# Kernel optimization log

Measured on AMD Instinct MI355X. Metric: run time of the kernel, lower is better.

## Reference

```python
import jax, jax.numpy as jnp
import numpy as np
from jax import lax

N_G, E_G, E_LG = 100000, 400000, 1200000
N_T, E_T, E_LGT = 50000, 100000, 300000
D_F, D_MSG_G = 64, 128
VOCAB, D_EMB, D_MSG_T = 780, 128, 128
N_ITERS_G, N_ITERS_T = 4, 4
SCALE = 0.05  # keep relu/sum chains numerically tame over iterations


def setup_inputs() -> dict:
    key = jax.random.key(0)
    ks = jax.random.split(key, 32)
    f32 = jnp.float32
    w = lambda k, sh: jax.random.normal(k, sh, f32) * SCALE
    return {
        "G_f": jax.random.normal(ks[0], (N_G, D_F), f32),
        "G_ef": jax.random.normal(ks[1], (E_G, D_F), f32),
        "G_src": jax.random.randint(ks[2], (E_G,), 0, N_G, jnp.int32),
        "G_dst": jax.random.randint(ks[3], (E_G,), 0, N_G, jnp.int32),
        "G_lg_src": jax.random.randint(ks[4], (E_LG,), 0, E_G, jnp.int32),
        "G_lg_dst": jax.random.randint(ks[5], (E_LG,), 0, E_G, jnp.int32),
        "T_id": jax.random.randint(ks[6], (N_T,), 0, VOCAB, jnp.int32),
        "T_src": jax.random.randint(ks[7], (E_T,), 0, N_T, jnp.int32),
        "T_dst": jax.random.randint(ks[8], (E_T,), 0, N_T, jnp.int32),
        "T_lg_src": jax.random.randint(ks[9], (E_LGT,), 0, E_T, jnp.int32),
        "T_lg_dst": jax.random.randint(ks[10], (E_LGT,), 0, E_T, jnp.int32),
        "embeddings": jax.random.normal(ks[11], (VOCAB, D_EMB), f32),
        "W1": w(ks[12], (D_F, D_MSG_G)),
        "W2": w(ks[13], (D_F, D_MSG_G)),
        "W3": w(ks[14], (D_MSG_G, D_MSG_G)),
        "U1_G": w(ks[15], (D_F, D_MSG_G)),
        "U2_G": w(ks[16], (D_MSG_G, D_MSG_G)),
        "Wz": w(ks[17], (D_EMB, D_MSG_T)),
        "Uz": w(ks[18], (D_MSG_T, D_MSG_T)),
        "Wr": w(ks[19], (D_EMB, D_MSG_T)),
        "Ur": w(ks[20], (D_MSG_T, D_MSG_T)),
        "Wh": w(ks[21], (D_EMB, D_MSG_T)),
        "Uh": w(ks[22], (D_MSG_T, D_MSG_T)),
        "U1_T": w(ks[23], (D_EMB, D_MSG_T)),
        "U2_T": w(ks[24], (D_MSG_T, D_MSG_T)),
    }


def reference(G_f, G_ef, G_src, G_dst, G_lg_src, G_lg_dst,
              T_id, T_src, T_dst, T_lg_src, T_lg_dst,
              embeddings, W1, W2, W3, U1_G, U2_G,
              Wz, Uz, Wr, Ur, Wh, Uh, U1_T, U2_T):
    seg = jax.ops.segment_sum

    # ---- molecule graph G: loopy-BP MLP messages on the line graph ----
    f_src_G = G_f[G_src]                               # [E_G, D_F] copy_src
    base_G = f_src_G @ W1 + G_ef @ W2                  # loop-invariant part of g1_G

    def stepG(msg, _):
        sum_msg = seg(msg[G_lg_src], G_lg_dst, num_segments=E_G)
        return jax.nn.relu(base_G + sum_msg @ W3), None

    msgG0 = jnp.zeros((E_G, D_MSG_G), G_f.dtype)
    msgG, _ = lax.scan(stepG, msgG0, None, length=N_ITERS_G)

    # readout g2_G: sum edge msgs into dst nodes
    sG = seg(msgG, G_dst, num_segments=N_G)
    x_G = jax.nn.relu(G_f @ U1_G + sG @ U2_G)          # [N_G, D_MSG_G]

    # ---- junction tree T: GRU messages on the tree line graph ----
    f_T = embeddings[T_id]                             # one-hot id @ embeddings
    f_src_T = f_T[T_src]                               # [E_T, D_EMB]
    xz, xr, xh = f_src_T @ Wz, f_src_T @ Wr, f_src_T @ Wh

    def stepT(msg, _):
        s = seg(msg[T_lg_src], T_lg_dst, num_segments=E_T)
        z = jax.nn.sigmoid(xz + s @ Uz)
        r = jax.nn.sigmoid(xr + s @ Ur)
        h = jnp.tanh(xh + (r * s) @ Uh)
        return (1.0 - z) * s + z * h, None

    msgT0 = jnp.zeros((E_T, D_MSG_T), f_T.dtype)
    msgT, _ = lax.scan(stepT, msgT0, None, length=N_ITERS_T)

    sT = seg(msgT, T_dst, num_segments=N_T)
    x_T = jax.nn.relu(f_T @ U1_T + sT @ U2_T)          # [N_T, D_MSG_T]

    # concat node readouts (same width) so output is a single array
    return jnp.concatenate([x_G, x_T], axis=0)         # [N_G+N_T, 128]
```

## Files before the change

kernel.cpp:

```cpp
#include <hip/hip_runtime.h>

#define NG 100000
#define EG 400000
#define ELG 1200000
#define NT 50000
#define ET 100000
#define ELGT 300000

#define GEG ((EG + 63) / 64)
#define GET ((ET + 63) / 64)
#define GNG ((NG + 63) / 64)
#define GNT ((NT + 63) / 64)

#define SEG1 EG
#define SEG2 (EG + NG)
#define SEG3 (EG + NG + ET)
#define NSEG_ALL (EG + NG + ET + NT)
#define NE_ALL (ELG + EG + ELGT + ET)

typedef unsigned short u16;
typedef unsigned int u32;
typedef __attribute__((ext_vector_type(8))) short bf16x8;
typedef __attribute__((ext_vector_type(4))) float f32x4;

#define TILE_BYTES (64 * 256)

__device__ __forceinline__ float bflo(u32 p){ return __uint_as_float(p << 16); }
__device__ __forceinline__ float bfhi(u32 p){ return __uint_as_float(p & 0xffff0000u); }
__device__ __forceinline__ float bf2f(u16 h){ return __uint_as_float(((u32)h) << 16); }
__device__ __forceinline__ u16 f2bf(float f){
  u32 u = __float_as_uint(f);
  u32 r = u + 0x7fffu + ((u >> 16) & 1u);
  return (u16)(r >> 16);
}
__device__ __forceinline__ float sigm(float x){ return 1.0f / (1.0f + __expf(-x)); }
__device__ __forceinline__ float tanh_(float x){ return 2.0f / (1.0f + __expf(-2.0f * x)) - 1.0f; }
__device__ __forceinline__ float relu_(float x){ return x > 0.0f ? x : 0.0f; }

__device__ __forceinline__ int swz(int r, int c){ return r * 256 + (c ^ ((r & 7) << 4)); }

__device__ __forceinline__ void zero8(float v[8]){
  #pragma unroll
  for (int j = 0; j < 8; j++) v[j] = 0.f;
}
__device__ __forceinline__ uint4 pack8(const float v[8]){
  uint4 o;
  o.x = f2bf(v[0]) | ((u32)f2bf(v[1]) << 16);
  o.y = f2bf(v[2]) | ((u32)f2bf(v[3]) << 16);
  o.z = f2bf(v[4]) | ((u32)f2bf(v[5]) << 16);
  o.w = f2bf(v[6]) | ((u32)f2bf(v[7]) << 16);
  return o;
}
__device__ __forceinline__ uint2 pack4(const f32x4& a){
  uint2 o;
  o.x = (u32)f2bf(a[0]) | ((u32)f2bf(a[1]) << 16);
  o.y = (u32)f2bf(a[2]) | ((u32)f2bf(a[3]) << 16);
  return o;
}

__global__ void k_sniff(const u32* __restrict__ g, int* __restrict__ flag){
  __shared__ int sh[2];
  if (threadIdx.x < 2) sh[threadIdx.x] = 0;
  __syncthreads();
  int c0 = 0, c1 = 0;
  for (int i = 0; i < 16; i++){
    u32 w = g[threadIdx.x * 16 + i];
    u32 lo = w & 0xFFFFu;
    if (lo == 0u) c0++;
    else { u32 e = (lo >> 7) & 0xFFu; if (e >= 96u && e <= 144u) c1++; }
  }
  atomicAdd(&sh[0], c0); atomicAdd(&sh[1], c1);
  __syncthreads();
  if (threadIdx.x == 0) *flag = (sh[0] < 512 && sh[1] > 2048) ? 1 : 0;
}

__global__ void k_cvt_all(const void* p0, const void* p1, const void* p2, const void* p3,
                          const void* p4, const void* p5, const void* p6, const void* p7,
                          const void* p8, const void* p9, const void* p10, const void* p11,
                          const void* p12, float* __restrict__ wm, const int* __restrict__ flagp){
  int i = blockIdx.x * 256 + threadIdx.x;
  if (i >= 188416) return;
  const int offs[14] = {0,8192,16384,32768,40960,57344,73728,90112,106496,122880,139264,155648,172032,188416};
  const void* ps[13] = {p0,p1,p2,p3,p4,p5,p6,p7,p8,p9,p10,p11,p12};
  int w = 0;
  while (i >= offs[w + 1]) w++;
  int li = i - offs[w];
  wm[i] = (*flagp) ? bf2f(((const u16*)ps[w])[li]) : ((const float*)ps[w])[li];
}

__global__ void k_mkfrag_all(const float* __restrict__ wm, u16* __restrict__ frag){
  const int wmo[13] = {0,8192,16384,32768,40960,57344,73728,90112,106496,122880,139264,155648,172032};
  const int nks[13] = {2,2,4,2,4,4,4,4,4,4,4,4,4};
  int b = blockIdx.x;
  int wi = 0, ks = b;
  while (ks >= nks[wi]){ ks -= nks[wi]; wi++; }
  const float* W = wm + wmo[wi];
  int nt = threadIdx.x >> 6, lane = threadIdx.x & 63;
  int kr = ks * 32 + ((lane >> 4) << 3);
  int col = nt * 16 + (lane & 15);
  u16* o = frag + (size_t)b * 4096 + nt * 512 + lane * 8;
  #pragma unroll
  for (int j = 0; j < 8; j++) o[j] = f2bf(W[(size_t)(kr + j) * 128 + col]);
}

__device__ __forceinline__ const void* rowdt(const void* mat, size_t row, int W, int bf){
  return bf ? (const void*)((const u16*)mat + row * (size_t)W)
            : (const void*)((const float*)mat + row * (size_t)W);
}
__device__ __forceinline__ void load8(const void* rowbase, int c8, int bf, float v[8]){
  if (bf){
    uint4 d = ((const uint4*)rowbase)[c8];
    v[0]=bflo(d.x); v[1]=bfhi(d.x); v[2]=bflo(d.y); v[3]=bfhi(d.y);
    v[4]=bflo(d.z); v[5]=bfhi(d.z); v[6]=bflo(d.w); v[7]=bfhi(d.w);
  } else {
    const float4* p = (const float4*)rowbase + (c8 << 1);
    float4 a = p[0], b = p[1];
    v[0]=a.x; v[1]=a.y; v[2]=a.z; v[3]=a.w; v[4]=b.x; v[5]=b.y; v[6]=b.z; v[7]=b.w;
  }
}

__global__ void k_hist_all(const int* __restrict__ Glgd, const int* __restrict__ Gd,
                           const int* __restrict__ Tlgd, const int* __restrict__ Td,
                           int* __restrict__ cnt){
  int e = blockIdx.x * 256 + threadIdx.x;
  if (e >= NE_ALL) return;
  int seg;
  if (e < ELG)                       seg = Glgd[e];
  else if (e < ELG + EG)             seg = SEG1 + Gd[e - ELG];
  else if (e < ELG + EG + ELGT)      seg = SEG2 + Tlgd[e - ELG - EG];
  else                               seg = SEG3 + Td[e - ELG - EG - ELGT];
  atomicAdd(&cnt[seg], 1);
}

__global__ void k_scan1(const int* __restrict__ cnt, int n, int* __restrict__ csum){
  int base = blockIdx.x * 4096, tid = threadIdx.x;
  int s = 0;
  for (int i = 0; i < 16; i++){ int idx = base + i * 256 + tid; if (idx < n) s += cnt[idx]; }
  __shared__ int red[4];
  for (int off = 32; off; off >>= 1) s += __shfl_down(s, off, 64);
  if ((tid & 63) == 0) red[tid >> 6] = s;
  __syncthreads();
  if (tid == 0) csum[blockIdx.x] = red[0] + red[1] + red[2] + red[3];
}

__global__ void k_scan2(int* csum, int nch, int* rowptr, int n){
  if (threadIdx.x == 0){
    int run = 0;
    for (int c = 0; c < nch; c++){ int t = csum[c]; csum[c] = run; run += t; }
    rowptr[n] = run;
  }
}

__global__ void k_scan3(const int* __restrict__ cnt, int n, const int* __restrict__ csum,
                        int* __restrict__ rowptr){
  __shared__ int buf[4096];
  __shared__ int tsum[256];
  int base = blockIdx.x * 4096, tid = threadIdx.x;
  for (int i = 0; i < 16; i++){ int idx = base + i * 256 + tid; buf[i * 256 + tid] = (idx < n) ? cnt[idx] : 0; }
  __syncthreads();
  int run = 0;
  for (int i = 0; i < 16; i++){ int v = buf[tid * 16 + i]; buf[tid * 16 + i] = run; run += v; }
  tsum[tid] = run;
  __syncthreads();
  for (int off = 1; off < 256; off <<= 1){
    int v = (tid >= off) ? tsum[tid - off] : 0;
    __syncthreads();
    tsum[tid] += v;
    __syncthreads();
  }
  int texcl = tsum[tid] - run;
  int cbase = csum[blockIdx.x];
  for (int i = 0; i < 16; i++){
    int idx = base + tid * 16 + i;
    if (idx < n) rowptr[idx] = cbase + texcl + buf[tid * 16 + i];
  }
}

__global__ void k_fill_all(const int* __restrict__ Glgd, const int* __restrict__ Glgs,
                           const int* __restrict__ Gd,
                           const int* __restrict__ Tlgd, const int* __restrict__ Tlgs,
                           const int* __restrict__ Td,
                           const int* __restrict__ rowptr, int* __restrict__ fill,
                           int* __restrict__ col){
  int e = blockIdx.x * 256 + threadIdx.x;
  if (e >= NE_ALL) return;
  int seg, srcv;
  if (e < ELG){                      seg = Glgd[e];                          srcv = Glgs[e]; }
  else if (e < ELG + EG){            int l = e - ELG;                        seg = SEG1 + Gd[l];  srcv = l; }
  else if (e < ELG + EG + ELGT){     int l = e - ELG - EG;                   seg = SEG2 + Tlgd[l]; srcv = Tlgs[l]; }
  else {                             int l = e - ELG - EG - ELGT;            seg = SEG3 + Td[l];  srcv = l; }
  int pos = atomicAdd(&fill[seg], 1);
  col[rowptr[seg] + pos] = srcv;
}


__device__ __forceinline__ void gather_tile(char* __restrict__ tile,
    const int* __restrict__ rowptr, const int* __restrict__ colidx,
    const u16* __restrict__ msg, int row0, int M)
{
  int tid = threadIdx.x;
  int rl = tid >> 2, q = tid & 3;
  int row = row0 + rl;
  float acc[4][8];
  #pragma unroll
  for (int v = 0; v < 4; v++) zero8(acc[v]);
  if (row < M){
    int p = rowptr[row], pe = rowptr[row + 1];
    for (; p < pe; ++p){
      int sr = colidx[p];
      const uint4* b = (const uint4*)(msg + (size_t)sr * 128);
      #pragma unroll
      for (int v = 0; v < 4; v++){
        uint4 d = b[v * 4 + q];
        acc[v][0] += bflo(d.x); acc[v][1] += bfhi(d.x);
        acc[v][2] += bflo(d.y); acc[v][3] += bfhi(d.y);
        acc[v][4] += bflo(d.z); acc[v][5] += bfhi(d.z);
        acc[v][6] += bflo(d.w); acc[v][7] += bfhi(d.w);
      }
    }
  }
  #pragma unroll
  for (int v = 0; v < 4; v++)
    *(uint4*)(tile + swz(rl, (v * 4 + q) * 16)) = pack8(acc[v]);
}

__device__ __forceinline__ void stage_cat_tile(char* __restrict__ tile,
    const void* __restrict__ Gf, const void* __restrict__ Gef,
    const int* __restrict__ Gsrc, int row0, int M, int bf)
{
  int tid = threadIdx.x, rl = tid >> 2, q = tid & 3;
  int row = row0 + rl;
  float A0[8], A1[8], B0[8], B1[8];
  if (row < M){
    int sr = Gsrc[row];
    const void* ra = rowdt(Gf, (size_t)sr, 64, bf);
    const void* rb = rowdt(Gef, (size_t)row, 64, bf);
    load8(ra, q, bf, A0); load8(ra, q + 4, bf, A1);
    load8(rb, q, bf, B0); load8(rb, q + 4, bf, B1);
  } else { zero8(A0); zero8(A1); zero8(B0); zero8(B1); }
  *(uint4*)(tile + swz(rl, q * 16))             = pack8(A0);
  *(uint4*)(tile + swz(rl, (q + 4) * 16))       = pack8(A1);
  *(uint4*)(tile + swz(rl, 128 + q * 16))       = pack8(B0);
  *(uint4*)(tile + swz(rl, 128 + (q + 4) * 16)) = pack8(B1);
}

__device__ __forceinline__ void stage_w64_tile(char* __restrict__ tile,
    const void* __restrict__ mat, int row0, int M, int bf)
{
  int tid = threadIdx.x, rl = tid >> 2, q = tid & 3;
  int row = row0 + rl;
  float A0[8], A1[8];
  if (row < M){
    const void* ra = rowdt(mat, (size_t)row, 64, bf);
    load8(ra, q, bf, A0); load8(ra, q + 4, bf, A1);
  } else { zero8(A0); zero8(A1); }
  *(uint4*)(tile + swz(rl, q * 16))       = pack8(A0);
  *(uint4*)(tile + swz(rl, (q + 4) * 16)) = pack8(A1);
}

__device__ __forceinline__ void stage_emb_tile(char* __restrict__ tile,
    const void* __restrict__ emb, const int* __restrict__ Tid,
    const int* __restrict__ idx, int row0, int M, int bf)
{
  int tid = threadIdx.x, rl = tid >> 2, q = tid & 3;
  int row = row0 + rl;
  if (row < M){
    int n = idx ? idx[row] : row;
    int id = Tid[n];
    const void* rb = rowdt(emb, (size_t)id, 128, bf);
    #pragma unroll
    for (int v = 0; v < 4; v++){
      float t[8]; load8(rb, v * 4 + q, bf, t);
      *(uint4*)(tile + swz(rl, (v * 4 + q) * 16)) = pack8(t);
    }
  } else {
    uint4 z = make_uint4(0, 0, 0, 0);
    #pragma unroll
    for (int v = 0; v < 4; v++)
      *(uint4*)(tile + swz(rl, (v * 4 + q) * 16)) = z;
  }
}

__device__ __forceinline__ void mma_acc(const char* __restrict__ tile, int stripe,
    const u16* __restrict__ frag, int ksteps, f32x4 (&acc)[8])
{
  int lane = threadIdx.x & 63;
  int ar = stripe + (lane & 15);
  int acb = (lane >> 4) << 4;
  for (int ks = 0; ks < ksteps; ks++){
    bf16x8 a = *(const bf16x8*)(tile + swz(ar, ks * 64 + acb));
    const u16* fb = frag + (size_t)ks * 4096 + lane * 8;
    #pragma unroll
    for (int nt = 0; nt < 8; nt++){
      bf16x8 b = *(const bf16x8*)(fb + (size_t)nt * 512);
      acc[nt] = __builtin_amdgcn_mfma_f32_16x16x32_bf16(a, b, acc[nt], 0, 0, 0);
    }
  }
}

#define INIT_ACC(A) { _Pragma("unroll") for (int n_=0;n_<8;n_++){ A[n_][0]=0.f; A[n_][1]=0.f; A[n_][2]=0.f; A[n_][3]=0.f; } }

__device__ __forceinline__ void repack_store(const char* __restrict__ tile,
    u16* __restrict__ dst, int row0, int M)
{
  int rl = threadIdx.x >> 2, q = threadIdx.x & 3;
  int grow = row0 + rl;
  if (grow < M){
    #pragma unroll
    for (int v = 0; v < 4; v++){
      uint4 d = *(const uint4*)(tile + swz(rl, (v * 4 + q) * 16));
      *(uint4*)(dst + (size_t)grow * 128 + (size_t)(v * 4 + q) * 8) = d;
    }
  }
}

__device__ __forceinline__ size_t fslot(int blk, int w, int nt){
  return ((((size_t)blk * 4 + w) * 8 + nt) * 64 + (threadIdx.x & 63)) * 4;
}


__global__ __launch_bounds__(256) void k_init(
    const void* __restrict__ Gf, const void* __restrict__ Gef, const int* __restrict__ Gsrc,
    const u16* __restrict__ fWcat, const int* __restrict__ flagp, u16* __restrict__ msgG,
    const void* __restrict__ emb, const int* __restrict__ Tid, const int* __restrict__ Tsrc,
    const u16* __restrict__ fWz, const u16* __restrict__ fWr, const u16* __restrict__ fWh,
    u16* __restrict__ xzf, u16* __restrict__ xrf, u16* __restrict__ xhf, u16* __restrict__ msgT)
{
  __shared__ char t0[TILE_BYTES];
  int bf = *flagp;
  int w = threadIdx.x >> 6, lane = threadIdx.x & 63, stripe = w * 16;
  if (blockIdx.x < GEG){
    int row0 = blockIdx.x * 64;
    stage_cat_tile(t0, Gf, Gef, Gsrc, row0, EG, bf);
    __syncthreads();
    f32x4 acc[8]; INIT_ACC(acc);
    mma_acc(t0, stripe, fWcat, 4, acc);
    #pragma unroll
    for (int nt = 0; nt < 8; nt++)
      #pragma unroll
      for (int r = 0; r < 4; r++){
        int rt = stripe + ((lane >> 4) << 2) + r;
        int cb = nt * 32 + (lane & 15) * 2;
        *(u16*)(t0 + swz(rt, cb)) = f2bf(relu_(acc[nt][r]));
      }
    __syncthreads();
    repack_store(t0, msgG, row0, EG);
  } else {
    int blk = blockIdx.x - GEG;
    int row0 = blk * 64;
    stage_emb_tile(t0, emb, Tid, Tsrc, row0, ET, bf);
    __syncthreads();
    f32x4 aZ[8]; INIT_ACC(aZ);
    mma_acc(t0, stripe, fWz, 4, aZ);
    {
      f32x4 aR[8]; INIT_ACC(aR);
      mma_acc(t0, stripe, fWr, 4, aR);
      #pragma unroll
      for (int nt = 0; nt < 8; nt++)
        *(uint2*)(xrf + fslot(blk, w, nt)) = pack4(aR[nt]);
    }
    f32x4 aH[8]; INIT_ACC(aH);
    mma_acc(t0, stripe, fWh, 4, aH);
    #pragma unroll
    for (int nt = 0; nt < 8; nt++){
      *(uint2*)(xzf + fslot(blk, w, nt)) = pack4(aZ[nt]);
      *(uint2*)(xhf + fslot(blk, w, nt)) = pack4(aH[nt]);
      #pragma unroll
      for (int r = 0; r < 4; r++){
        int rt = stripe + ((lane >> 4) << 2) + r;
        int cb = nt * 32 + (lane & 15) * 2;
        *(u16*)(t0 + swz(rt, cb)) = f2bf(sigm(aZ[nt][r]) * tanh_(aH[nt][r]));
      }
    }
    __syncthreads();
    repack_store(t0, msgT, row0, ET);
  }
}

__global__ __launch_bounds__(256) void k_iter(
    const u16* __restrict__ msgInG, u16* __restrict__ msgOutG,
    const void* __restrict__ Gf, const void* __restrict__ Gef, const int* __restrict__ Gsrc,
    const int* __restrict__ rp, const int* __restrict__ col,
    const u16* __restrict__ fWcat, const u16* __restrict__ fW3, const int* __restrict__ flagp,
    const u16* __restrict__ msgInT, u16* __restrict__ msgOutT,
    const u16* __restrict__ fUz, const u16* __restrict__ fUr, const u16* __restrict__ fUh,
    const u16* __restrict__ xzf, const u16* __restrict__ xrf, const u16* __restrict__ xhf)
{
  __shared__ char t0[TILE_BYTES];
  __shared__ char t1[TILE_BYTES];
  int w = threadIdx.x >> 6, lane = threadIdx.x & 63, stripe = w * 16;
  if (blockIdx.x < GEG){
    int bf = *flagp;
    int row0 = blockIdx.x * 64;
    stage_cat_tile(t0, Gf, Gef, Gsrc, row0, EG, bf);
    gather_tile(t1, rp, col, msgInG, row0, EG);
    __syncthreads();
    f32x4 acc[8]; INIT_ACC(acc);
    mma_acc(t0, stripe, fWcat, 4, acc);
    mma_acc(t1, stripe, fW3, 4, acc);
    #pragma unroll
    for (int nt = 0; nt < 8; nt++)
      #pragma unroll
      for (int r = 0; r < 4; r++){
        int rt = stripe + ((lane >> 4) << 2) + r;
        int cb = nt * 32 + (lane & 15) * 2;
        *(u16*)(t1 + swz(rt, cb)) = f2bf(relu_(acc[nt][r]));
      }
    __syncthreads();
    repack_store(t1, msgOutG, row0, EG);
  } else {
    int blk = blockIdx.x - GEG;
    int row0 = blk * 64;
    gather_tile(t0, rp + SEG2, col, msgInT, row0, ET);
    __syncthreads();
    f32x4 aZ[8], aR[8];
    INIT_ACC(aZ); INIT_ACC(aR);
    mma_acc(t0, stripe, fUz, 4, aZ);
    mma_acc(t0, stripe, fUr, 4, aR);
    float zz[8][4];
    #pragma unroll
    for (int nt = 0; nt < 8; nt++){
      uint2 z4 = *(const uint2*)(xzf + fslot(blk, w, nt));
      uint2 r4 = *(const uint2*)(xrf + fslot(blk, w, nt));
      float xzv[4] = {bflo(z4.x), bfhi(z4.x), bflo(z4.y), bfhi(z4.y)};
      float xrv[4] = {bflo(r4.x), bfhi(r4.x), bflo(r4.y), bfhi(r4.y)};
      #pragma unroll
      for (int r = 0; r < 4; r++){
        int rt = stripe + ((lane >> 4) << 2) + r;
        int cb = nt * 32 + (lane & 15) * 2;
        float s = bf2f(*(const u16*)(t0 + swz(rt, cb)));
        float z = sigm(xzv[r] + aZ[nt][r]);
        float rr = sigm(xrv[r] + aR[nt][r]);
        zz[nt][r] = z;
        *(u16*)(t1 + swz(rt, cb)) = f2bf(rr * s);
      }
    }
    __syncthreads();
    f32x4 aH[8]; INIT_ACC(aH);
    mma_acc(t1, stripe, fUh, 4, aH);
    #pragma unroll
    for (int nt = 0; nt < 8; nt++){
      uint2 h4 = *(const uint2*)(xhf + fslot(blk, w, nt));
      float xhv[4] = {bflo(h4.x), bfhi(h4.x), bflo(h4.y), bfhi(h4.y)};
      #pragma unroll
      for (int r = 0; r < 4; r++){
        int rt = stripe + ((lane >> 4) << 2) + r;
        int cb = nt * 32 + (lane & 15) * 2;
        float s = bf2f(*(const u16*)(t0 + swz(rt, cb)));
        float h = tanh_(xhv[r] + aH[nt][r]);
        float m = (1.f - zz[nt][r]) * s + zz[nt][r] * h;
        *(u16*)(t0 + swz(rt, cb)) = f2bf(m);
      }
    }
    __syncthreads();
    repack_store(t0, msgOutT, row0, ET);
  }
}

__global__ __launch_bounds__(256) void k_readout(
    const void* __restrict__ Gf, const u16* __restrict__ msgG,
    const int* __restrict__ rp, const int* __restrict__ col,
    const u16* __restrict__ fU1G, const u16* __restrict__ fU2G,
    const void* __restrict__ emb, const int* __restrict__ Tid, const u16* __restrict__ msgT,
    const u16* __restrict__ fU1T, const u16* __restrict__ fU2T,
    const int* __restrict__ flagp, float* __restrict__ out)
{
  __shared__ char t0[TILE_BYTES];
  __shared__ char t1[TILE_BYTES];
  int bf = *flagp;
  int w = threadIdx.x >> 6, lane = threadIdx.x & 63, stripe = w * 16;
  if (blockIdx.x < GNG){
    int row0 = blockIdx.x * 64;
    stage_w64_tile(t0, Gf, row0, NG, bf);
    gather_tile(t1, rp + SEG1, col, msgG, row0, NG);
    __syncthreads();
    f32x4 acc[8]; INIT_ACC(acc);
    mma_acc(t0, stripe, fU1G, 2, acc);
    mma_acc(t1, stripe, fU2G, 4, acc);
    #pragma unroll
    for (int nt = 0; nt < 8; nt++)
      #pragma unroll
      for (int r = 0; r < 4; r++){
        int R = row0 + stripe + ((lane >> 4) << 2) + r;
        if (R < NG) out[(size_t)R * 128 + nt * 16 + (lane & 15)] = relu_(acc[nt][r]);
      }
  } else {
    int row0 = (blockIdx.x - GNG) * 64;
    stage_emb_tile(t0, emb, Tid, nullptr, row0, NT, bf);
    gather_tile(t1, rp + SEG3, col, msgT, row0, NT);
    __syncthreads();
    f32x4 acc[8]; INIT_ACC(acc);
    mma_acc(t0, stripe, fU1T, 4, acc);
    mma_acc(t1, stripe, fU2T, 4, acc);
    #pragma unroll
    for (int nt = 0; nt < 8; nt++)
      #pragma unroll
      for (int r = 0; r < 4; r++){
        int R = row0 + stripe + ((lane >> 4) << 2) + r;
        if (R < NT) out[(size_t)(NG + R) * 128 + nt * 16 + (lane & 15)] = relu_(acc[nt][r]);
      }
  }
}

extern "C" void kernel_launch(void* const* d_in, const int* in_sizes, int n_in,
                              void* d_out, int out_size, void* d_ws, size_t ws_size,
                              hipStream_t stream)
{
  const void* G_f      = d_in[0];
  const void* G_ef     = d_in[1];
  const int*  G_src    = (const int*)d_in[2];
  const int*  G_dst    = (const int*)d_in[3];
  const int*  G_lg_src = (const int*)d_in[4];
  const int*  G_lg_dst = (const int*)d_in[5];
  const int*  T_id     = (const int*)d_in[6];
  const int*  T_src    = (const int*)d_in[7];
  const int*  T_dst    = (const int*)d_in[8];
  const int*  T_lg_src = (const int*)d_in[9];
  const int*  T_lg_dst = (const int*)d_in[10];
  const void* emb      = d_in[11];
  float* out = (float*)d_out;
  (void)in_sizes; (void)n_in; (void)out_size; (void)ws_size;

  size_t off = 0;
  auto alloc = [&](size_t bytes) -> char* {
    char* p = (char*)d_ws + off;
    off += (bytes + 255) & ~(size_t)255;
    return p;
  };

  int*   flag = (int*)alloc(256);
  float* wm   = (float*)alloc(sizeof(float) * 188416);
  u16*   frag = (u16*)alloc(2 * 46 * 4096);
  const u16* fWcat = frag;
  const u16* fW3   = frag + (size_t)4  * 4096;
  const u16* fU1G  = frag + (size_t)8  * 4096;
  const u16* fU2G  = frag + (size_t)10 * 4096;
  const u16* fWz   = frag + (size_t)14 * 4096;
  const u16* fUz   = frag + (size_t)18 * 4096;
  const u16* fWr   = frag + (size_t)22 * 4096;
  const u16* fUr   = frag + (size_t)26 * 4096;
  const u16* fWh   = frag + (size_t)30 * 4096;
  const u16* fUh   = frag + (size_t)34 * 4096;
  const u16* fU1T  = frag + (size_t)38 * 4096;
  const u16* fU2T  = frag + (size_t)42 * 4096;

  int* rp   = (int*)alloc(sizeof(int) * (NSEG_ALL + 1));
  int* col  = (int*)alloc(sizeof(int) * NE_ALL);
  int* cnt  = (int*)alloc(sizeof(int) * 2 * NSEG_ALL);
  int* csum = (int*)alloc(sizeof(int) * 256);
  u16* msgGA = (u16*)alloc((size_t)EG * 128 * 2);
  u16* msgGB = (u16*)alloc((size_t)EG * 128 * 2);
  u16* xzf   = (u16*)alloc((size_t)GET * 8192 * 2);
  u16* xrf   = (u16*)alloc((size_t)GET * 8192 * 2);
  u16* xhf   = (u16*)alloc((size_t)GET * 8192 * 2);
  u16* msgTA = (u16*)alloc((size_t)ET * 128 * 2);
  u16* msgTB = (u16*)alloc((size_t)ET * 128 * 2);

  k_sniff<<<1, 256, 0, stream>>>((const u32*)G_ef, flag);
  k_cvt_all<<<(188416 + 255) / 256, 256, 0, stream>>>(
      d_in[12], d_in[13], d_in[14], d_in[15], d_in[16], d_in[17], d_in[18],
      d_in[19], d_in[20], d_in[21], d_in[22], d_in[23], d_in[24], wm, flag);
  k_mkfrag_all<<<46, 512, 0, stream>>>(wm, frag);

  hipMemsetAsync(cnt, 0, sizeof(int) * 2 * NSEG_ALL, stream);
  k_hist_all<<<(NE_ALL + 255) / 256, 256, 0, stream>>>(G_lg_dst, G_dst, T_lg_dst, T_dst, cnt);
  int nch = (NSEG_ALL + 4095) / 4096;
  k_scan1<<<nch, 256, 0, stream>>>(cnt, NSEG_ALL, csum);
  k_scan2<<<1, 64, 0, stream>>>(csum, nch, rp, NSEG_ALL);
  k_scan3<<<nch, 256, 0, stream>>>(cnt, NSEG_ALL, csum, rp);
  k_fill_all<<<(NE_ALL + 255) / 256, 256, 0, stream>>>(
      G_lg_dst, G_lg_src, G_dst, T_lg_dst, T_lg_src, T_dst, rp, cnt + NSEG_ALL, col);

  k_init<<<GEG + GET, 256, 0, stream>>>(G_f, G_ef, G_src, fWcat, flag, msgGA,
                                        emb, T_id, T_src, fWz, fWr, fWh, xzf, xrf, xhf, msgTA);
  k_iter<<<GEG + GET, 256, 0, stream>>>(msgGA, msgGB, G_f, G_ef, G_src, rp, col, fWcat, fW3, flag,
                                        msgTA, msgTB, fUz, fUr, fUh, xzf, xrf, xhf);
  k_iter<<<GEG + GET, 256, 0, stream>>>(msgGB, msgGA, G_f, G_ef, G_src, rp, col, fWcat, fW3, flag,
                                        msgTB, msgTA, fUz, fUr, fUh, xzf, xrf, xhf);
  k_iter<<<GEG + GET, 256, 0, stream>>>(msgGA, msgGB, G_f, G_ef, G_src, rp, col, fWcat, fW3, flag,
                                        msgTA, msgTB, fUz, fUr, fUh, xzf, xrf, xhf);
  k_readout<<<GNG + GNT, 256, 0, stream>>>(G_f, msgGB, rp, col, fU1G, fU2G,
                                           emb, T_id, msgTB, fU1T, fU2T, flag, out);
}
```

Measured before the change: 1.351 ms.

## Load MFMA A-fragments directly to registers and drop block-wide LDS staging

Each lane now gathers and sums its neighbour messages straight into the MFMA A-operand layout and builds bf16 fragments in registers, so the shared-memory staging tiles and most block barriers go away. Barriers become wave-level fences, because each wave now only touches its own 16-row stripe of the tile. The gather loop is unrolled by two to keep more loads in flight. The GRU step carries z and (1-z)*s as packed values instead of re-reading s. Block order is changed so the smaller tree blocks launch first, and LDS use drops from two tiles to one, which raises possible occupancy.

```diff
diff --git a/kernel.cpp b/kernel.cpp
--- a/kernel.cpp
+++ b/kernel.cpp
@@ -23,7 +23,7 @@
 typedef __attribute__((ext_vector_type(8))) short bf16x8;
 typedef __attribute__((ext_vector_type(4))) float f32x4;
 
-#define TILE_BYTES (64 * 256)
+#define TILE_B 16384
 
 __device__ __forceinline__ float bflo(u32 p){ return __uint_as_float(p << 16); }
 __device__ __forceinline__ float bfhi(u32 p){ return __uint_as_float(p & 0xffff0000u); }
@@ -36,6 +36,7 @@
 __device__ __forceinline__ float sigm(float x){ return 1.0f / (1.0f + __expf(-x)); }
 __device__ __forceinline__ float tanh_(float x){ return 2.0f / (1.0f + __expf(-2.0f * x)) - 1.0f; }
 __device__ __forceinline__ float relu_(float x){ return x > 0.0f ? x : 0.0f; }
+__device__ __forceinline__ void wfence(){ __builtin_amdgcn_wave_barrier(); }
 
 __device__ __forceinline__ int swz(int r, int c){ return r * 256 + (c ^ ((r & 7) << 4)); }
 
@@ -56,6 +57,24 @@
   o.x = (u32)f2bf(a[0]) | ((u32)f2bf(a[1]) << 16);
   o.y = (u32)f2bf(a[2]) | ((u32)f2bf(a[3]) << 16);
   return o;
+}
+__device__ __forceinline__ uint2 pack4a(const float v[4]){
+  uint2 o;
+  o.x = (u32)f2bf(v[0]) | ((u32)f2bf(v[1]) << 16);
+  o.y = (u32)f2bf(v[2]) | ((u32)f2bf(v[3]) << 16);
+  return o;
+}
+__device__ __forceinline__ void unp4(uint2 u, float v[4]){
+  v[0] = bflo(u.x); v[1] = bfhi(u.x); v[2] = bflo(u.y); v[3] = bfhi(u.y);
+}
+__device__ __forceinline__ bf16x8 packfrag(const float v[8]){
+  union { uint4 u; bf16x8 b; } c; c.u = pack8(v); return c.b;
+}
+__device__ __forceinline__ bf16x8 zfrag(){
+  union { uint4 u; bf16x8 b; } c; c.u = make_uint4(0, 0, 0, 0); return c.b;
+}
+__device__ __forceinline__ bf16x8 as_frag(uint4 u){
+  union { uint4 u; bf16x8 b; } c; c.u = u; return c.b;
 }
 
 __global__ void k_sniff(const u32* __restrict__ g, int* __restrict__ flag){
@@ -185,115 +204,58 @@
   int e = blockIdx.x * 256 + threadIdx.x;
   if (e >= NE_ALL) return;
   int seg, srcv;
-  if (e < ELG){                      seg = Glgd[e];                          srcv = Glgs[e]; }
-  else if (e < ELG + EG){            int l = e - ELG;                        seg = SEG1 + Gd[l];  srcv = l; }
-  else if (e < ELG + EG + ELGT){     int l = e - ELG - EG;                   seg = SEG2 + Tlgd[l]; srcv = Tlgs[l]; }
-  else {                             int l = e - ELG - EG - ELGT;            seg = SEG3 + Td[l];  srcv = l; }
+  if (e < ELG){                      seg = Glgd[e];                           srcv = Glgs[e]; }
+  else if (e < ELG + EG){            int l = e - ELG;                         seg = SEG1 + Gd[l];   srcv = l; }
+  else if (e < ELG + EG + ELGT){     int l = e - ELG - EG;                    seg = SEG2 + Tlgd[l]; srcv = Tlgs[l]; }
+  else {                             int l = e - ELG - EG - ELGT;             seg = SEG3 + Td[l];   srcv = l; }
   int pos = atomicAdd(&fill[seg], 1);
   col[rowptr[seg] + pos] = srcv;
 }
 
 
-__device__ __forceinline__ void gather_tile(char* __restrict__ tile,
-    const int* __restrict__ rowptr, const int* __restrict__ colidx,
-    const u16* __restrict__ msg, int row0, int M)
-{
-  int tid = threadIdx.x;
-  int rl = tid >> 2, q = tid & 3;
-  int row = row0 + rl;
-  float acc[4][8];
+__device__ __forceinline__ void acc8_add(float (&a)[8], uint4 d){
+  a[0] += bflo(d.x); a[1] += bfhi(d.x);
+  a[2] += bflo(d.y); a[3] += bfhi(d.y);
+  a[4] += bflo(d.z); a[5] += bfhi(d.z);
+  a[6] += bflo(d.w); a[7] += bfhi(d.w);
+}
+
+__device__ __forceinline__ void gather_accum(const int* __restrict__ rowptr,
+    const int* __restrict__ colidx, const u16* __restrict__ msg,
+    int row, int M, int kg, float (&acc)[4][8])
+{
   #pragma unroll
-  for (int v = 0; v < 4; v++) zero8(acc[v]);
-  if (row < M){
-    int p = rowptr[row], pe = rowptr[row + 1];
-    for (; p < pe; ++p){
-      int sr = colidx[p];
-      const uint4* b = (const uint4*)(msg + (size_t)sr * 128);
-      #pragma unroll
-      for (int v = 0; v < 4; v++){
-        uint4 d = b[v * 4 + q];
-        acc[v][0] += bflo(d.x); acc[v][1] += bfhi(d.x);
-        acc[v][2] += bflo(d.y); acc[v][3] += bfhi(d.y);
-        acc[v][4] += bflo(d.z); acc[v][5] += bfhi(d.z);
-        acc[v][6] += bflo(d.w); acc[v][7] += bfhi(d.w);
-      }
-    }
-  }
+  for (int ks = 0; ks < 4; ks++) zero8(acc[ks]);
+  if (row >= M) return;
+  int p = rowptr[row], pe = rowptr[row + 1];
+  for (; p + 1 < pe; p += 2){
+    const uint4* b0 = (const uint4*)(msg + (size_t)colidx[p] * 128);
+    const uint4* b1 = (const uint4*)(msg + (size_t)colidx[p + 1] * 128);
+    uint4 v0[4], v1[4];
+    #pragma unroll
+    for (int ks = 0; ks < 4; ks++){ v0[ks] = b0[ks * 4 + kg]; v1[ks] = b1[ks * 4 + kg]; }
+    #pragma unroll
+    for (int ks = 0; ks < 4; ks++){ acc8_add(acc[ks], v0[ks]); acc8_add(acc[ks], v1[ks]); }
+  }
+  if (p < pe){
+    const uint4* b0 = (const uint4*)(msg + (size_t)colidx[p] * 128);
+    #pragma unroll
+    for (int ks = 0; ks < 4; ks++){ uint4 v = b0[ks * 4 + kg]; acc8_add(acc[ks], v); }
+  }
+}
+
+template<int KS>
+__device__ __forceinline__ void mma_f(const bf16x8* a, const u16* __restrict__ frag,
+                                      f32x4 (&acc)[8])
+{
+  int lane = threadIdx.x & 63;
   #pragma unroll
-  for (int v = 0; v < 4; v++)
-    *(uint4*)(tile + swz(rl, (v * 4 + q) * 16)) = pack8(acc[v]);
-}
-
-__device__ __forceinline__ void stage_cat_tile(char* __restrict__ tile,
-    const void* __restrict__ Gf, const void* __restrict__ Gef,
-    const int* __restrict__ Gsrc, int row0, int M, int bf)
-{
-  int tid = threadIdx.x, rl = tid >> 2, q = tid & 3;
-  int row = row0 + rl;
-  float A0[8], A1[8], B0[8], B1[8];
-  if (row < M){
-    int sr = Gsrc[row];
-    const void* ra = rowdt(Gf, (size_t)sr, 64, bf);
-    const void* rb = rowdt(Gef, (size_t)row, 64, bf);
-    load8(ra, q, bf, A0); load8(ra, q + 4, bf, A1);
-    load8(rb, q, bf, B0); load8(rb, q + 4, bf, B1);
-  } else { zero8(A0); zero8(A1); zero8(B0); zero8(B1); }
-  *(uint4*)(tile + swz(rl, q * 16))             = pack8(A0);
-  *(uint4*)(tile + swz(rl, (q + 4) * 16))       = pack8(A1);
-  *(uint4*)(tile + swz(rl, 128 + q * 16))       = pack8(B0);
-  *(uint4*)(tile + swz(rl, 128 + (q + 4) * 16)) = pack8(B1);
-}
-
-__device__ __forceinline__ void stage_w64_tile(char* __restrict__ tile,
-    const void* __restrict__ mat, int row0, int M, int bf)
-{
-  int tid = threadIdx.x, rl = tid >> 2, q = tid & 3;
-  int row = row0 + rl;
-  float A0[8], A1[8];
-  if (row < M){
-    const void* ra = rowdt(mat, (size_t)row, 64, bf);
-    load8(ra, q, bf, A0); load8(ra, q + 4, bf, A1);
-  } else { zero8(A0); zero8(A1); }
-  *(uint4*)(tile + swz(rl, q * 16))       = pack8(A0);
-  *(uint4*)(tile + swz(rl, (q + 4) * 16)) = pack8(A1);
-}
-
-__device__ __forceinline__ void stage_emb_tile(char* __restrict__ tile,
-    const void* __restrict__ emb, const int* __restrict__ Tid,
-    const int* __restrict__ idx, int row0, int M, int bf)
-{
-  int tid = threadIdx.x, rl = tid >> 2, q = tid & 3;
-  int row = row0 + rl;
-  if (row < M){
-    int n = idx ? idx[row] : row;
-    int id = Tid[n];
-    const void* rb = rowdt(emb, (size_t)id, 128, bf);
-    #pragma unroll
-    for (int v = 0; v < 4; v++){
-      float t[8]; load8(rb, v * 4 + q, bf, t);
-      *(uint4*)(tile + swz(rl, (v * 4 + q) * 16)) = pack8(t);
-    }
-  } else {
-    uint4 z = make_uint4(0, 0, 0, 0);
-    #pragma unroll
-    for (int v = 0; v < 4; v++)
-      *(uint4*)(tile + swz(rl, (v * 4 + q) * 16)) = z;
-  }
-}
-
-__device__ __forceinline__ void mma_acc(const char* __restrict__ tile, int stripe,
-    const u16* __restrict__ frag, int ksteps, f32x4 (&acc)[8])
-{
-  int lane = threadIdx.x & 63;
-  int ar = stripe + (lane & 15);
-  int acb = (lane >> 4) << 4;
-  for (int ks = 0; ks < ksteps; ks++){
-    bf16x8 a = *(const bf16x8*)(tile + swz(ar, ks * 64 + acb));
+  for (int ks = 0; ks < KS; ks++){
     const u16* fb = frag + (size_t)ks * 4096 + lane * 8;
     #pragma unroll
     for (int nt = 0; nt < 8; nt++){
       bf16x8 b = *(const bf16x8*)(fb + (size_t)nt * 512);
-      acc[nt] = __builtin_amdgcn_mfma_f32_16x16x32_bf16(a, b, acc[nt], 0, 0, 0);
+      acc[nt] = __builtin_amdgcn_mfma_f32_16x16x32_bf16(a[ks], b, acc[nt], 0, 0, 0);
     }
   }
 }
@@ -316,6 +278,25 @@
 
 __device__ __forceinline__ size_t fslot(int blk, int w, int nt){
   return ((((size_t)blk * 4 + w) * 8 + nt) * 64 + (threadIdx.x & 63)) * 4;
+}
+
+__device__ __forceinline__ void load_catfrag(const void* __restrict__ Gf,
+    const void* __restrict__ Gef, const int* __restrict__ Gsrc,
+    int arow, int kg, int bf, bf16x8 (&fC)[4])
+{
+  if (arow < EG){
+    int sr = Gsrc[arow];
+    const void* ra = rowdt(Gf, (size_t)sr, 64, bf);
+    const void* rb = rowdt(Gef, (size_t)arow, 64, bf);
+    float t[8];
+    load8(ra, kg, bf, t);     fC[0] = packfrag(t);
+    load8(ra, 4 + kg, bf, t); fC[1] = packfrag(t);
+    load8(rb, kg, bf, t);     fC[2] = packfrag(t);
+    load8(rb, 4 + kg, bf, t); fC[3] = packfrag(t);
+  } else {
+    #pragma unroll
+    for (int ks = 0; ks < 4; ks++) fC[ks] = zfrag();
+  }
 }
 
 
@@ -326,54 +307,62 @@
     const u16* __restrict__ fWz, const u16* __restrict__ fWr, const u16* __restrict__ fWh,
     u16* __restrict__ xzf, u16* __restrict__ xrf, u16* __restrict__ xhf, u16* __restrict__ msgT)
 {
-  __shared__ char t0[TILE_BYTES];
+  __shared__ char t0[TILE_B];
   int bf = *flagp;
-  int w = threadIdx.x >> 6, lane = threadIdx.x & 63, stripe = w * 16;
-  if (blockIdx.x < GEG){
-    int row0 = blockIdx.x * 64;
-    stage_cat_tile(t0, Gf, Gef, Gsrc, row0, EG, bf);
-    __syncthreads();
-    f32x4 acc[8]; INIT_ACC(acc);
-    mma_acc(t0, stripe, fWcat, 4, acc);
-    #pragma unroll
-    for (int nt = 0; nt < 8; nt++)
-      #pragma unroll
-      for (int r = 0; r < 4; r++){
-        int rt = stripe + ((lane >> 4) << 2) + r;
-        int cb = nt * 32 + (lane & 15) * 2;
-        *(u16*)(t0 + swz(rt, cb)) = f2bf(relu_(acc[nt][r]));
-      }
-    __syncthreads();
-    repack_store(t0, msgG, row0, EG);
-  } else {
-    int blk = blockIdx.x - GEG;
-    int row0 = blk * 64;
-    stage_emb_tile(t0, emb, Tid, Tsrc, row0, ET, bf);
-    __syncthreads();
-    f32x4 aZ[8]; INIT_ACC(aZ);
-    mma_acc(t0, stripe, fWz, 4, aZ);
-    {
-      f32x4 aR[8]; INIT_ACC(aR);
-      mma_acc(t0, stripe, fWr, 4, aR);
-      #pragma unroll
-      for (int nt = 0; nt < 8; nt++)
-        *(uint2*)(xrf + fslot(blk, w, nt)) = pack4(aR[nt]);
-    }
-    f32x4 aH[8]; INIT_ACC(aH);
-    mma_acc(t0, stripe, fWh, 4, aH);
+  int lane = threadIdx.x & 63, w = threadIdx.x >> 6;
+  int stripe = w * 16, kg = lane >> 4, m16 = lane & 15;
+  if (blockIdx.x < GET){
+    int blk = blockIdx.x, row0 = blk * 64, arow = row0 + stripe + m16;
+    bf16x8 fE[4];
+    if (arow < ET){
+      int id = Tid[Tsrc[arow]];
+      const void* rb = rowdt(emb, (size_t)id, 128, bf);
+      #pragma unroll
+      for (int ks = 0; ks < 4; ks++){
+        float t[8]; load8(rb, ks * 4 + kg, bf, t); fE[ks] = packfrag(t);
+      }
+    } else {
+      #pragma unroll
+      for (int ks = 0; ks < 4; ks++) fE[ks] = zfrag();
+    }
+    f32x4 aZ[8], aR[8]; INIT_ACC(aZ); INIT_ACC(aR);
+    mma_f<4>(fE, fWz, aZ);
+    mma_f<4>(fE, fWr, aR);
     #pragma unroll
     for (int nt = 0; nt < 8; nt++){
       *(uint2*)(xzf + fslot(blk, w, nt)) = pack4(aZ[nt]);
+      *(uint2*)(xrf + fslot(blk, w, nt)) = pack4(aR[nt]);
+    }
+    f32x4 aH[8]; INIT_ACC(aH);
+    mma_f<4>(fE, fWh, aH);
+    #pragma unroll
+    for (int nt = 0; nt < 8; nt++){
       *(uint2*)(xhf + fslot(blk, w, nt)) = pack4(aH[nt]);
       #pragma unroll
       for (int r = 0; r < 4; r++){
-        int rt = stripe + ((lane >> 4) << 2) + r;
-        int cb = nt * 32 + (lane & 15) * 2;
+        int rt = stripe + (kg << 2) + r;
+        int cb = nt * 32 + m16 * 2;
         *(u16*)(t0 + swz(rt, cb)) = f2bf(sigm(aZ[nt][r]) * tanh_(aH[nt][r]));
       }
     }
-    __syncthreads();
+    wfence();
     repack_store(t0, msgT, row0, ET);
+  } else {
+    int blk = blockIdx.x - GET, row0 = blk * 64, arow = row0 + stripe + m16;
+    bf16x8 fC[4];
+    load_catfrag(Gf, Gef, Gsrc, arow, kg, bf, fC);
+    f32x4 acc[8]; INIT_ACC(acc);
+    mma_f<4>(fC, fWcat, acc);
+    #pragma unroll
+    for (int nt = 0; nt < 8; nt++)
+      #pragma unroll
+      for (int r = 0; r < 4; r++){
+        int rt = stripe + (kg << 2) + r;
+        int cb = nt * 32 + m16 * 2;
+        *(u16*)(t0 + swz(rt, cb)) = f2bf(relu_(acc[nt][r]));
+      }
+    wfence();
+    repack_store(t0, msgG, row0, EG);
   }
 }
 
@@ -386,74 +375,91 @@
     const u16* __restrict__ fUz, const u16* __restrict__ fUr, const u16* __restrict__ fUh,
     const u16* __restrict__ xzf, const u16* __restrict__ xrf, const u16* __restrict__ xhf)
 {
-  __shared__ char t0[TILE_BYTES];
-  __shared__ char t1[TILE_BYTES];
-  int w = threadIdx.x >> 6, lane = threadIdx.x & 63, stripe = w * 16;
-  if (blockIdx.x < GEG){
-    int bf = *flagp;
-    int row0 = blockIdx.x * 64;
-    stage_cat_tile(t0, Gf, Gef, Gsrc, row0, EG, bf);
-    gather_tile(t1, rp, col, msgInG, row0, EG);
-    __syncthreads();
-    f32x4 acc[8]; INIT_ACC(acc);
-    mma_acc(t0, stripe, fWcat, 4, acc);
-    mma_acc(t1, stripe, fW3, 4, acc);
-    #pragma unroll
-    for (int nt = 0; nt < 8; nt++)
-      #pragma unroll
-      for (int r = 0; r < 4; r++){
-        int rt = stripe + ((lane >> 4) << 2) + r;
-        int cb = nt * 32 + (lane & 15) * 2;
-        *(u16*)(t1 + swz(rt, cb)) = f2bf(relu_(acc[nt][r]));
-      }
-    __syncthreads();
-    repack_store(t1, msgOutG, row0, EG);
-  } else {
-    int blk = blockIdx.x - GEG;
-    int row0 = blk * 64;
-    gather_tile(t0, rp + SEG2, col, msgInT, row0, ET);
-    __syncthreads();
-    f32x4 aZ[8], aR[8];
-    INIT_ACC(aZ); INIT_ACC(aR);
-    mma_acc(t0, stripe, fUz, 4, aZ);
-    mma_acc(t0, stripe, fUr, 4, aR);
-    float zz[8][4];
+  __shared__ char t0[TILE_B];
+  int lane = threadIdx.x & 63, w = threadIdx.x >> 6;
+  int stripe = w * 16, kg = lane >> 4, m16 = lane & 15;
+  if (blockIdx.x < GET){
+    int blk = blockIdx.x, row0 = blk * 64, arow = row0 + stripe + m16;
+    float ga[4][8];
+    gather_accum(rp + SEG2, col, msgInT, arow, ET, kg, ga);
+    bf16x8 fS[4];
+    #pragma unroll
+    for (int ks = 0; ks < 4; ks++){
+      uint4 pk = pack8(ga[ks]);
+      *(uint4*)(t0 + swz(stripe + m16, ks * 64 + kg * 16)) = pk;
+      fS[ks] = as_frag(pk);
+    }
+    f32x4 aZ[8], aR[8]; INIT_ACC(aZ); INIT_ACC(aR);
+    mma_f<4>(fS, fUz, aZ);
+    mma_f<4>(fS, fUr, aR);
+    wfence();
+    uint2 zpk[8], wpk[8];
     #pragma unroll
     for (int nt = 0; nt < 8; nt++){
       uint2 z4 = *(const uint2*)(xzf + fslot(blk, w, nt));
       uint2 r4 = *(const uint2*)(xrf + fslot(blk, w, nt));
-      float xzv[4] = {bflo(z4.x), bfhi(z4.x), bflo(z4.y), bfhi(z4.y)};
-      float xrv[4] = {bflo(r4.x), bfhi(r4.x), bflo(r4.y), bfhi(r4.y)};
+      float xzv[4], xrv[4], zv[4], wv[4];
+      unp4(z4, xzv); unp4(r4, xrv);
       #pragma unroll
       for (int r = 0; r < 4; r++){
-        int rt = stripe + ((lane >> 4) << 2) + r;
-        int cb = nt * 32 + (lane & 15) * 2;
+        int rt = stripe + (kg << 2) + r;
+        int cb = nt * 32 + m16 * 2;
         float s = bf2f(*(const u16*)(t0 + swz(rt, cb)));
         float z = sigm(xzv[r] + aZ[nt][r]);
         float rr = sigm(xrv[r] + aR[nt][r]);
-        zz[nt][r] = z;
-        *(u16*)(t1 + swz(rt, cb)) = f2bf(rr * s);
-      }
-    }
-    __syncthreads();
+        zv[r] = z;
+        wv[r] = s * (1.f - z);
+        *(u16*)(t0 + swz(rt, cb)) = f2bf(rr * s);
+      }
+      zpk[nt] = pack4a(zv); wpk[nt] = pack4a(wv);
+    }
+    wfence();
+    bf16x8 fRS[4];
+    #pragma unroll
+    for (int ks = 0; ks < 4; ks++)
+      fRS[ks] = *(const bf16x8*)(t0 + swz(stripe + m16, ks * 64 + kg * 16));
     f32x4 aH[8]; INIT_ACC(aH);
-    mma_acc(t1, stripe, fUh, 4, aH);
+    mma_f<4>(fRS, fUh, aH);
+    wfence();
     #pragma unroll
     for (int nt = 0; nt < 8; nt++){
       uint2 h4 = *(const uint2*)(xhf + fslot(blk, w, nt));
-      float xhv[4] = {bflo(h4.x), bfhi(h4.x), bflo(h4.y), bfhi(h4.y)};
+      float xhv[4], zv[4], wv[4];
+      unp4(h4, xhv); unp4(zpk[nt], zv); unp4(wpk[nt], wv);
       #pragma unroll
       for (int r = 0; r < 4; r++){
-        int rt = stripe + ((lane >> 4) << 2) + r;
-        int cb = nt * 32 + (lane & 15) * 2;
-        float s = bf2f(*(const u16*)(t0 + swz(rt, cb)));
         float h = tanh_(xhv[r] + aH[nt][r]);
-        float m = (1.f - zz[nt][r]) * s + zz[nt][r] * h;
+        float m = wv[r] + zv[r] * h;
+        int rt = stripe + (kg << 2) + r;
+        int cb = nt * 32 + m16 * 2;
         *(u16*)(t0 + swz(rt, cb)) = f2bf(m);
       }
     }
-    __syncthreads();
+    wfence();
     repack_store(t0, msgOutT, row0, ET);
+  } else {
+    int bf = *flagp;
+    int blk = blockIdx.x - GET, row0 = blk * 64, arow = row0 + stripe + m16;
+    bf16x8 fC[4];
+    load_catfrag(Gf, Gef, Gsrc, arow, kg, bf, fC);
+    float ga[4][8];
+    gather_accum(rp, col, msgInG, arow, EG, kg, ga);
+    bf16x8 fS[4];
+    #pragma unroll
+    for (int ks = 0; ks < 4; ks++) fS[ks] = packfrag(ga[ks]);
+    f32x4 acc[8]; INIT_ACC(acc);
+    mma_f<4>(fS, fW3, acc);
+    mma_f<4>(fC, fWcat, acc);
+    #pragma unroll
+    for (int nt = 0; nt < 8; nt++)
+      #pragma unroll
+      for (int r = 0; r < 4; r++){
+        int rt = stripe + (kg << 2) + r;
+        int cb = nt * 32 + m16 * 2;
+        *(u16*)(t0 + swz(rt, cb)) = f2bf(relu_(acc[nt][r]));
+      }
+    wfence();
+    repack_store(t0, msgOutG, row0, EG);
   }
 }
 
@@ -465,39 +471,61 @@
     const u16* __restrict__ fU1T, const u16* __restrict__ fU2T,
     const int* __restrict__ flagp, float* __restrict__ out)
 {
-  __shared__ char t0[TILE_BYTES];
-  __shared__ char t1[TILE_BYTES];
   int bf = *flagp;
-  int w = threadIdx.x >> 6, lane = threadIdx.x & 63, stripe = w * 16;
-  if (blockIdx.x < GNG){
-    int row0 = blockIdx.x * 64;
-    stage_w64_tile(t0, Gf, row0, NG, bf);
-    gather_tile(t1, rp + SEG1, col, msgG, row0, NG);
-    __syncthreads();
+  int lane = threadIdx.x & 63, w = threadIdx.x >> 6;
+  int stripe = w * 16, kg = lane >> 4, m16 = lane & 15;
+  if (blockIdx.x < GNT){
+    int row0 = blockIdx.x * 64, arow = row0 + stripe + m16;
+    bf16x8 fE[4];
+    if (arow < NT){
+      int id = Tid[arow];
+      const void* rb = rowdt(emb, (size_t)id, 128, bf);
+      #pragma unroll
+      for (int ks = 0; ks < 4; ks++){
+        float t[8]; load8(rb, ks * 4 + kg, bf, t); fE[ks] = packfrag(t);
+      }
+    } else {
+      #pragma unroll
+      for (int ks = 0; ks < 4; ks++) fE[ks] = zfrag();
+    }
+    float ga[4][8];
+    gather_accum(rp + SEG3, col, msgT, arow, NT, kg, ga);
+    bf16x8 fS[4];
+    #pragma unroll
+    for (int ks = 0; ks < 4; ks++) fS[ks] = packfrag(ga[ks]);
     f32x4 acc[8]; INIT_ACC(acc);
-    mma_acc(t0, stripe, fU1G, 2, acc);
-    mma_acc(t1, stripe, fU2G, 4, acc);
+    mma_f<4>(fE, fU1T, acc);
+    mma_f<4>(fS, fU2T, acc);
     #pragma unroll
     for (int nt = 0; nt < 8; nt++)
       #pragma unroll
       for (int r = 0; r < 4; r++){
-        int R = row0 + stripe + ((lane >> 4) << 2) + r;
-        if (R < NG) out[(size_t)R * 128 + nt * 16 + (lane & 15)] = relu_(acc[nt][r]);
+        int R = row0 + stripe + (kg << 2) + r;
+        if (R < NT) out[(size_t)(NG + R) * 128 + nt * 16 + m16] = relu_(acc[nt][r]);
       }
   } else {
-    int row0 = (blockIdx.x - GNG) * 64;
-    stage_emb_tile(t0, emb, Tid, nullptr, row0, NT, bf);
-    gather_tile(t1, rp + SEG3, col, msgT, row0, NT);
-    __syncthreads();
+    int row0 = (blockIdx.x - GNT) * 64, arow = row0 + stripe + m16;
+    bf16x8 fG[2];
+    if (arow < NG){
+      const void* ra = rowdt(Gf, (size_t)arow, 64, bf);
+      float t[8];
+      load8(ra, kg, bf, t);     fG[0] = packfrag(t);
+      load8(ra, 4 + kg, bf, t); fG[1] = packfrag(t);
+    } else { fG[0] = zfrag(); fG[1] = zfrag(); }
+    float ga[4][8];
+    gather_accum(rp + SEG1, col, msgG, arow, NG, kg, ga);
+    bf16x8 fS[4];
+    #pragma unroll
+    for (int ks = 0; ks < 4; ks++) fS[ks] = packfrag(ga[ks]);
     f32x4 acc[8]; INIT_ACC(acc);
-    mma_acc(t0, stripe, fU1T, 4, acc);
-    mma_acc(t1, stripe, fU2T, 4, acc);
+    mma_f<2>(fG, fU1G, acc);
+    mma_f<4>(fS, fU2G, acc);
     #pragma unroll
     for (int nt = 0; nt < 8; nt++)
       #pragma unroll
       for (int r = 0; r < 4; r++){
-        int R = row0 + stripe + ((lane >> 4) << 2) + r;
-        if (R < NT) out[(size_t)(NG + R) * 128 + nt * 16 + (lane & 15)] = relu_(acc[nt][r]);
+        int R = row0 + stripe + (kg << 2) + r;
+        if (R < NG) out[(size_t)R * 128 + nt * 16 + m16] = relu_(acc[nt][r]);
       }
   }
 }
@@ -571,14 +599,14 @@
   k_fill_all<<<(NE_ALL + 255) / 256, 256, 0, stream>>>(
       G_lg_dst, G_lg_src, G_dst, T_lg_dst, T_lg_src, T_dst, rp, cnt + NSEG_ALL, col);
 
-  k_init<<<GEG + GET, 256, 0, stream>>>(G_f, G_ef, G_src, fWcat, flag, msgGA,
+  k_init<<<GET + GEG, 256, 0, stream>>>(G_f, G_ef, G_src, fWcat, flag, msgGA,
                                         emb, T_id, T_src, fWz, fWr, fWh, xzf, xrf, xhf, msgTA);
-  k_iter<<<GEG + GET, 256, 0, stream>>>(msgGA, msgGB, G_f, G_ef, G_src, rp, col, fWcat, fW3, flag,
+  k_iter<<<GET + GEG, 256, 0, stream>>>(msgGA, msgGB, G_f, G_ef, G_src, rp, col, fWcat, fW3, flag,
                                         msgTA, msgTB, fUz, fUr, fUh, xzf, xrf, xhf);
-  k_iter<<<GEG + GET, 256, 0, stream>>>(msgGB, msgGA, G_f, G_ef, G_src, rp, col, fWcat, fW3, flag,
+  k_iter<<<GET + GEG, 256, 0, stream>>>(msgGB, msgGA, G_f, G_ef, G_src, rp, col, fWcat, fW3, flag,
                                         msgTB, msgTA, fUz, fUr, fUh, xzf, xrf, xhf);
-  k_iter<<<GEG + GET, 256, 0, stream>>>(msgGA, msgGB, G_f, G_ef, G_src, rp, col, fWcat, fW3, flag,
+  k_iter<<<GET + GEG, 256, 0, stream>>>(msgGA, msgGB, G_f, G_ef, G_src, rp, col, fWcat, fW3, flag,
                                         msgTA, msgTB, fUz, fUr, fUh, xzf, xrf, xhf);
-  k_readout<<<GNG + GNT, 256, 0, stream>>>(G_f, msgGB, rp, col, fU1G, fU2G,
+  k_readout<<<GNT + GNG, 256, 0, stream>>>(G_f, msgGB, rp, col, fU1G, fU2G,
                                            emb, T_id, msgTB, fU1T, fU2T, flag, out);
 }
```

Result: faster. 1.246 ms (-7.7%).
